# Kernel tuning notes

Measured on AMD Instinct MI355X. Metric: run time of the kernel, lower is better.

The kernel has to match this reference:

```python
import jax, jax.numpy as jnp
import numpy as np

MARGIN = 1.0
EPS = 1e-12  # safe sqrt/normalize clamp; used entries have magnitude >> EPS


def _normalize(x):
    return x / jnp.maximum(jnp.linalg.norm(x, axis=-1, keepdims=True), EPS)


def _cdist(x, y):
    # Pairwise L2 distances, matches torch.cdist(p=2)
    sq = (jnp.sum(x * x, axis=-1)[:, None]
          + jnp.sum(y * y, axis=-1)[None, :]
          - 2.0 * (x @ y.T))
    return jnp.sqrt(jnp.maximum(sq, EPS))


def setup_inputs() -> dict:
    key = jax.random.key(0)
    k1, k2, k3 = jax.random.split(key, 3)
    B, P, D = 4096, 2, 256
    anchor = jax.random.normal(k1, (B, D), dtype=jnp.float32)
    positive = jax.random.normal(k2, (B, P, D), dtype=jnp.float32)
    labels = jax.random.randint(k3, (B,), 0, 200)
    return {"anchor": anchor, "positive": positive, "labels": labels}


def reference(anchor, positive, labels):
    a = _normalize(anchor)            # [B, D]
    p = _normalize(positive)          # [B, P, D]
    B = a.shape[0]
    all_labels = jnp.concatenate([labels, labels])           # [2B]
    neg_mask = all_labels[None, :] != labels[:, None]        # [B, 2B]
    idx = jnp.arange(B)
    losses = []
    for v in range(p.shape[1]):  # loop over small fixed num_positives
        feats = jnp.concatenate([a, p[:, v]], axis=0)        # [2B, D]
        dist = _cdist(feats, feats)                          # [2B, 2B]
        pos_dist = dist[idx, idx + B]                        # [B]
        # hard negative mining: min distance over different-label columns
        neg_dist = jnp.min(jnp.where(neg_mask, dist[:B], jnp.inf), axis=1)  # [B]
        losses.append(jnp.maximum(pos_dist - neg_dist + MARGIN, 0.0))
    return jnp.mean(jnp.stack(losses))
```

## Files before the change

### kernel.cpp

```cpp
#include <hip/hip_runtime.h>
#include <hip/hip_bf16.h>

#define NB    4096
#define ND    256
#define NP    2
#define TOT   (NB * 3)
#define NCHUNK 48
#define COLS_PER_CHUNK 256
#define TILES 16
#define IMIN_SENT (-1073741824)
#define INV_SCALE (1.0f / 16129.0f)

typedef float f32x4 __attribute__((ext_vector_type(4)));
typedef int   i32x4 __attribute__((ext_vector_type(4)));

#define WS_F_OFF    0
#define WS_POS_OFF  (TOT * 256)
#define WS_NEG_OFF  (WS_POS_OFF + NB * NP * 4)

__global__ void norm_pos_kernel(const float* __restrict__ anchor,
                                const float* __restrict__ positive,
                                unsigned char* __restrict__ F2,
                                float* __restrict__ posArr,
                                int* __restrict__ negmax) {
    if (blockIdx.x < 48) negmax[blockIdx.x * 256 + threadIdx.x] = IMIN_SENT;

    int wid = threadIdx.x >> 6, lane = threadIdx.x & 63;
    int row = blockIdx.x * 4 + wid;
    int group = row >> 4, r15 = row & 15;
    int kk = lane >> 4, quad = (lane >> 2) & 3, jj = (lane & 3) * 4;
    int* dst = (int*)(F2 + (size_t)group * 4096 + kk * 1024 + (quad * 16 + r15) * 16 + jj);

    if (row < NB) {
        const float* src = anchor + (size_t)row * ND;
        float4 x = *(const float4*)(src + lane * 4);
        float ss = x.x * x.x + x.y * x.y + x.z * x.z + x.w * x.w;
        #pragma unroll
        for (int m = 1; m < 64; m <<= 1) ss += __shfl_xor(ss, m, 64);
        float inv = 127.0f / fmaxf(sqrtf(ss), 1e-12f);
        int b0 = (int)rintf(x.x * inv) & 0xff;
        int b1 = (int)rintf(x.y * inv) & 0xff;
        int b2 = (int)rintf(x.z * inv) & 0xff;
        int b3 = (int)rintf(x.w * inv) & 0xff;
        *dst = b0 | (b1 << 8) | (b2 << 16) | (b3 << 24);
    } else {
        int q = row - NB;
        int v = q >> 12;
        int j = q & (NB - 1);
        const float* sp = positive + (size_t)(j * NP + v) * ND;
        const float* sa = anchor + (size_t)j * ND;
        float4 xp = *(const float4*)(sp + lane * 4);
        float4 xa = *(const float4*)(sa + lane * 4);
        float sspv = xp.x * xp.x + xp.y * xp.y + xp.z * xp.z + xp.w * xp.w;
        float ssa  = xa.x * xa.x + xa.y * xa.y + xa.z * xa.z + xa.w * xa.w;
        float dot  = xa.x * xp.x + xa.y * xp.y + xa.z * xp.z + xa.w * xp.w;
        #pragma unroll
        for (int m = 1; m < 64; m <<= 1) {
            sspv += __shfl_xor(sspv, m, 64);
            ssa  += __shfl_xor(ssa, m, 64);
            dot  += __shfl_xor(dot, m, 64);
        }
        float invp = 127.0f / fmaxf(sqrtf(sspv), 1e-12f);
        int b0 = (int)rintf(xp.x * invp) & 0xff;
        int b1 = (int)rintf(xp.y * invp) & 0xff;
        int b2 = (int)rintf(xp.z * invp) & 0xff;
        int b3 = (int)rintf(xp.w * invp) & 0xff;
        *dst = b0 | (b1 << 8) | (b2 << 16) | (b3 << 24);
        if (lane == 0) {
            float inva = 1.0f / fmaxf(sqrtf(ssa), 1e-12f);
            float invpf = invp * (1.0f / 127.0f);
            float dn = dot * inva * invpf;
            float sq = 2.0f - 2.0f * dn;
            posArr[j * NP + v] = sqrtf(fmaxf(sq, 1e-12f));
        }
    }
}

__global__ __launch_bounds__(512) void gram_max_kernel(
        const unsigned char* __restrict__ F2,
        const int* __restrict__ labels,
        int* __restrict__ negmax) {
    __shared__ unsigned char ldsB[TILES * 4096];
    __shared__ int slab[COLS_PER_CHUNK];
    int tid = threadIdx.x;
    int wid = tid >> 6, lane = tid & 63;
    int l15 = lane & 15, quad = lane >> 4;

    int id = blockIdx.x;
    int chunk = id >> 4;
    int rbi   = id & 15;

    int rowBase = rbi * 256 + wid * 32;
    int col0 = chunk * COLS_PER_CHUNK;
    int part = chunk >> 4;

    {
        const unsigned char* src = F2 + (size_t)chunk * 65536 + (size_t)wid * 8192 + lane * 16;
        unsigned char* dst = ldsB + wid * 8192;
        #pragma unroll
        for (int j = 0; j < 8; ++j)
            __builtin_amdgcn_global_load_lds((const unsigned int*)(src + j * 1024),
                                             (unsigned int*)(dst + j * 1024), 16, 0, 0);
    }

    i32x4 af[2][4];
    #pragma unroll
    for (int s = 0; s < 2; ++s) {
        const unsigned char* ab = F2 + (size_t)(rbi * 16 + wid * 2 + s) * 4096 + lane * 16;
        #pragma unroll
        for (int kk = 0; kk < 4; ++kk)
            af[s][kk] = *(const i32x4*)(ab + kk * 1024);
    }
    unsigned rlp[2];
    #pragma unroll
    for (int s = 0; s < 2; ++s) {
        const int* lb = labels + rowBase + s * 16 + quad * 4;
        rlp[s] = (unsigned)lb[0] | ((unsigned)lb[1] << 8)
               | ((unsigned)lb[2] << 16) | ((unsigned)lb[3] << 24);
    }
    if (tid < COLS_PER_CHUNK) slab[tid] = labels[(col0 & (NB - 1)) + tid];

    int vmax[2][4];
    #pragma unroll
    for (int s = 0; s < 2; ++s)
        #pragma unroll
        for (int r = 0; r < 4; ++r) vmax[s][r] = IMIN_SENT;

    __syncthreads();

    #pragma unroll 2
    for (int ct = 0; ct < TILES; ++ct) {
        i32x4 bfr[4];
        #pragma unroll
        for (int kk = 0; kk < 4; ++kk)
            bfr[kk] = *(const i32x4*)&ldsB[ct * 4096 + kk * 1024 + lane * 16];

        int lc = slab[ct * 16 + l15];
        unsigned lcq = (unsigned)lc * 0x01010101u;

        i32x4 acc[2];
        #pragma unroll
        for (int s = 0; s < 2; ++s) acc[s] = (i32x4){0, 0, 0, 0};
        #pragma unroll
        for (int kk = 0; kk < 4; ++kk)
            #pragma unroll
            for (int s = 0; s < 2; ++s)
                acc[s] = __builtin_amdgcn_mfma_i32_16x16x64_i8(af[s][kk], bfr[kk], acc[s], 0, 0, 0);

        #pragma unroll
        for (int s = 0; s < 2; ++s) {
            unsigned x = rlp[s] ^ lcq;
            #pragma unroll
            for (int r = 0; r < 4; ++r) {
                bool neq = ((x >> (8 * r)) & 0xffu) != 0u;
                int cand = neq ? acc[s][r] : IMIN_SENT;
                vmax[s][r] = vmax[s][r] > cand ? vmax[s][r] : cand;
            }
        }
    }

    #pragma unroll
    for (int m = 1; m < 16; m <<= 1)
        #pragma unroll
        for (int s = 0; s < 2; ++s)
            #pragma unroll
            for (int r = 0; r < 4; ++r) {
                int o = __shfl_xor(vmax[s][r], m, 64);
                vmax[s][r] = vmax[s][r] > o ? vmax[s][r] : o;
            }

    if (l15 == 0) {
        #pragma unroll
        for (int s = 0; s < 2; ++s)
            #pragma unroll
            for (int r = 0; r < 4; ++r) {
                int row = rowBase + s * 16 + quad * 4 + r;
                atomicMax(&negmax[part * NB + row], vmax[s][r]);
            }
    }
}

__global__ void finalize_kernel(const int* __restrict__ negmax,
                                const float* __restrict__ posArr,
                                float* __restrict__ out) {
    int row = blockIdx.x * 256 + threadIdx.x;
    int ia = negmax[row];
    int i0 = negmax[NB + row];
    int i1 = negmax[2 * NB + row];
    int m0 = ia > i0 ? ia : i0;
    int m1 = ia > i1 ? ia : i1;
    float d0 = (float)m0 * INV_SCALE;
    float d1 = (float)m1 * INV_SCALE;
    float n0 = sqrtf(fmaxf(2.0f - 2.0f * d0, 1e-12f));
    float n1 = sqrtf(fmaxf(2.0f - 2.0f * d1, 1e-12f));
    float l = fmaxf(posArr[row * 2 + 0] - n0 + 1.0f, 0.0f)
            + fmaxf(posArr[row * 2 + 1] - n1 + 1.0f, 0.0f);
    int lane = threadIdx.x & 63, wid = threadIdx.x >> 6;
    #pragma unroll
    for (int m = 1; m < 64; m <<= 1) l += __shfl_xor(l, m, 64);
    __shared__ float wsum[4];
    if (lane == 0) wsum[wid] = l;
    __syncthreads();
    if (threadIdx.x == 0) {
        float s = wsum[0] + wsum[1] + wsum[2] + wsum[3];
        atomicAdd(out, s * (1.0f / (NB * NP)));
    }
}

extern "C" void kernel_launch(void* const* d_in, const int* in_sizes, int n_in,
                              void* d_out, int out_size, void* d_ws, size_t ws_size,
                              hipStream_t stream) {
    const float* anchor   = (const float*)d_in[0];
    const float* positive = (const float*)d_in[1];
    const int*   labels   = (const int*)d_in[2];
    float* out = (float*)d_out;

    unsigned char* F2 = (unsigned char*)((char*)d_ws + WS_F_OFF);
    float* posArr     = (float*)((char*)d_ws + WS_POS_OFF);
    int*   negmax     = (int*)((char*)d_ws + WS_NEG_OFF);

    hipMemsetAsync(d_out, 0, sizeof(float), stream);
    norm_pos_kernel<<<TOT / 4, 256, 0, stream>>>(anchor, positive, F2, posArr, negmax);
    gram_max_kernel<<<(NB / 256) * NCHUNK, 512, 0, stream>>>(F2, labels, negmax);
    finalize_kernel<<<NB / 256, 256, 0, stream>>>(negmax, posArr, out);
}
```

Baseline: 87.52 us.

## Fuse finalize into gram kernel via last-block counter and drop memset

Removes the separate finalize kernel and the output memset. The gram kernel now counts finished blocks with an atomic counter, and the last block to finish reads negmax and posArr with agent-scope loads, computes the loss and writes the output directly. The counter is reset in norm_pos_kernel, and the intermediate stores there become nontemporal. This saves two launches on the stream, at the cost of a serial tail in a single block and an extra fence plus atomic in every block.

```diff
diff --git a/kernel.cpp b/kernel.cpp
--- a/kernel.cpp
+++ b/kernel.cpp
@@ -17,13 +17,22 @@
 #define WS_F_OFF    0
 #define WS_POS_OFF  (TOT * 256)
 #define WS_NEG_OFF  (WS_POS_OFF + NB * NP * 4)
+#define WS_CNT_OFF  (WS_NEG_OFF + 3 * NB * 4)
+
+__device__ __forceinline__ int agent_load(const int* p) {
+    return __hip_atomic_load(p, __ATOMIC_RELAXED, __HIP_MEMORY_SCOPE_AGENT);
+}
 
 __global__ void norm_pos_kernel(const float* __restrict__ anchor,
                                 const float* __restrict__ positive,
                                 unsigned char* __restrict__ F2,
                                 float* __restrict__ posArr,
-                                int* __restrict__ negmax) {
-    if (blockIdx.x < 48) negmax[blockIdx.x * 256 + threadIdx.x] = IMIN_SENT;
+                                int* __restrict__ negmax,
+                                int* __restrict__ cnt) {
+    if (blockIdx.x < 48)
+        __builtin_nontemporal_store(IMIN_SENT, &negmax[blockIdx.x * 256 + threadIdx.x]);
+    if (blockIdx.x == 48 && threadIdx.x == 0)
+        __builtin_nontemporal_store(0, cnt);
 
     int wid = threadIdx.x >> 6, lane = threadIdx.x & 63;
     int row = blockIdx.x * 4 + wid;
@@ -42,7 +51,7 @@
         int b1 = (int)rintf(x.y * inv) & 0xff;
         int b2 = (int)rintf(x.z * inv) & 0xff;
         int b3 = (int)rintf(x.w * inv) & 0xff;
-        *dst = b0 | (b1 << 8) | (b2 << 16) | (b3 << 24);
+        __builtin_nontemporal_store(b0 | (b1 << 8) | (b2 << 16) | (b3 << 24), dst);
     } else {
         int q = row - NB;
         int v = q >> 12;
@@ -65,13 +74,13 @@
         int b1 = (int)rintf(xp.y * invp) & 0xff;
         int b2 = (int)rintf(xp.z * invp) & 0xff;
         int b3 = (int)rintf(xp.w * invp) & 0xff;
-        *dst = b0 | (b1 << 8) | (b2 << 16) | (b3 << 24);
+        __builtin_nontemporal_store(b0 | (b1 << 8) | (b2 << 16) | (b3 << 24), dst);
         if (lane == 0) {
             float inva = 1.0f / fmaxf(sqrtf(ssa), 1e-12f);
             float invpf = invp * (1.0f / 127.0f);
             float dn = dot * inva * invpf;
             float sq = 2.0f - 2.0f * dn;
-            posArr[j * NP + v] = sqrtf(fmaxf(sq, 1e-12f));
+            __builtin_nontemporal_store(sqrtf(fmaxf(sq, 1e-12f)), &posArr[j * NP + v]);
         }
     }
 }
@@ -79,9 +88,15 @@
 __global__ __launch_bounds__(512) void gram_max_kernel(
         const unsigned char* __restrict__ F2,
         const int* __restrict__ labels,
-        int* __restrict__ negmax) {
+        const float* __restrict__ posArr,
+        int* __restrict__ negmax,
+        int* __restrict__ cnt,
+        float* __restrict__ out) {
     __shared__ unsigned char ldsB[TILES * 4096];
     __shared__ int slab[COLS_PER_CHUNK];
+    __shared__ int lastFlag;
+    __shared__ float wsum[8];
+
     int tid = threadIdx.x;
     int wid = tid >> 6, lane = tid & 63;
     int l15 = lane & 15, quad = lane >> 4;
@@ -178,32 +193,41 @@
                 atomicMax(&negmax[part * NB + row], vmax[s][r]);
             }
     }
-}
-
-__global__ void finalize_kernel(const int* __restrict__ negmax,
-                                const float* __restrict__ posArr,
-                                float* __restrict__ out) {
-    int row = blockIdx.x * 256 + threadIdx.x;
-    int ia = negmax[row];
-    int i0 = negmax[NB + row];
-    int i1 = negmax[2 * NB + row];
-    int m0 = ia > i0 ? ia : i0;
-    int m1 = ia > i1 ? ia : i1;
-    float d0 = (float)m0 * INV_SCALE;
-    float d1 = (float)m1 * INV_SCALE;
-    float n0 = sqrtf(fmaxf(2.0f - 2.0f * d0, 1e-12f));
-    float n1 = sqrtf(fmaxf(2.0f - 2.0f * d1, 1e-12f));
-    float l = fmaxf(posArr[row * 2 + 0] - n0 + 1.0f, 0.0f)
-            + fmaxf(posArr[row * 2 + 1] - n1 + 1.0f, 0.0f);
-    int lane = threadIdx.x & 63, wid = threadIdx.x >> 6;
-    #pragma unroll
-    for (int m = 1; m < 64; m <<= 1) l += __shfl_xor(l, m, 64);
-    __shared__ float wsum[4];
-    if (lane == 0) wsum[wid] = l;
+
+    __threadfence();
+    if (tid == 0) {
+        int old = atomicAdd(cnt, 1);
+        lastFlag = (old == (int)gridDim.x - 1);
+    }
     __syncthreads();
-    if (threadIdx.x == 0) {
-        float s = wsum[0] + wsum[1] + wsum[2] + wsum[3];
-        atomicAdd(out, s * (1.0f / (NB * NP)));
+    if (!lastFlag) return;
+    __threadfence();
+
+    float lsum = 0.0f;
+    #pragma unroll
+    for (int k = 0; k < 8; ++k) {
+        int row = tid + k * 512;
+        int ia = agent_load(&negmax[row]);
+        int i0 = agent_load(&negmax[NB + row]);
+        int i1 = agent_load(&negmax[2 * NB + row]);
+        int m0 = ia > i0 ? ia : i0;
+        int m1 = ia > i1 ? ia : i1;
+        float d0 = (float)m0 * INV_SCALE;
+        float d1 = (float)m1 * INV_SCALE;
+        float n0 = sqrtf(fmaxf(2.0f - 2.0f * d0, 1e-12f));
+        float n1 = sqrtf(fmaxf(2.0f - 2.0f * d1, 1e-12f));
+        float2 pr = *(const float2*)&posArr[row * 2];
+        lsum += fmaxf(pr.x - n0 + 1.0f, 0.0f) + fmaxf(pr.y - n1 + 1.0f, 0.0f);
+    }
+    #pragma unroll
+    for (int m = 1; m < 64; m <<= 1) lsum += __shfl_xor(lsum, m, 64);
+    if (lane == 0) wsum[wid] = lsum;
+    __syncthreads();
+    if (tid == 0) {
+        float s = 0.0f;
+        #pragma unroll
+        for (int w = 0; w < 8; ++w) s += wsum[w];
+        out[0] = s * (1.0f / (NB * NP));
     }
 }
 
@@ -218,9 +242,8 @@
     unsigned char* F2 = (unsigned char*)((char*)d_ws + WS_F_OFF);
     float* posArr     = (float*)((char*)d_ws + WS_POS_OFF);
     int*   negmax     = (int*)((char*)d_ws + WS_NEG_OFF);
-
-    hipMemsetAsync(d_out, 0, sizeof(float), stream);
-    norm_pos_kernel<<<TOT / 4, 256, 0, stream>>>(anchor, positive, F2, posArr, negmax);
-    gram_max_kernel<<<(NB / 256) * NCHUNK, 512, 0, stream>>>(F2, labels, negmax);
-    finalize_kernel<<<NB / 256, 256, 0, stream>>>(negmax, posArr, out);
-}
+    int*   cnt        = (int*)((char*)d_ws + WS_CNT_OFF);
+
+    norm_pos_kernel<<<TOT / 4, 256, 0, stream>>>(anchor, positive, F2, posArr, negmax, cnt);
+    gram_max_kernel<<<(NB / 256) * NCHUNK, 512, 0, stream>>>(F2, labels, posArr, negmax, cnt, out);
+}
```

Result: slower. 171.0 us (+95.4%).
